# Performance work log

Hardware: AMD Instinct MI355X
Metric: run time of the kernel (lower is better)

Reference implementation:

```python
import jax, jax.numpy as jnp
import numpy as np

SPARSE_SHAPE = (41, 1600, 1408)  # (D, H, W), batch_size = 1
N_VOXELS = 200000
BN_EPS = 1e-3


def _kernel_offsets():
    # 27 offsets of a 3x3x3 kernel, padding=1 -> offsets in {-1,0,1}^3
    g = np.stack(np.meshgrid(*([np.arange(-1, 2)] * 3), indexing='ij'), axis=-1)
    return jnp.asarray(g.reshape(-1, 3), dtype=jnp.int32)  # (27, 3)


def _neighbor_map(coords):
    """Submanifold rulebook: for each active voxel and each of 27 offsets,
    index of the active neighbor voxel, or N (sentinel) if inactive/out-of-bounds."""
    D, H, W = SPARSE_SHAPE
    N = coords.shape[0]
    b, z, y, x = coords[:, 0], coords[:, 1], coords[:, 2], coords[:, 3]
    flat = ((b * D + z) * H + y) * W + x  # batch_size=1
    grid = jnp.full((D * H * W,), N, dtype=jnp.int32).at[flat].set(
        jnp.arange(N, dtype=jnp.int32))
    offs = _kernel_offsets()                      # (27, 3)
    nc = coords[:, None, 1:4] + offs[None]        # (N, 27, 3)
    lim = jnp.asarray([D, H, W], dtype=jnp.int32)
    valid = jnp.all((nc >= 0) & (nc < lim), axis=-1)  # (N, 27)
    nflat = ((b[:, None] * D + nc[..., 0]) * H + nc[..., 1]) * W + nc[..., 2]
    nbr = jnp.where(valid, grid[jnp.where(valid, nflat, 0)], N)
    return nbr  # (N, 27) int32, sentinel = N


def _subm_conv(features, nbr, w):
    # gather -> batched small GEMM -> (implicit) scatter back to same voxels
    pad = jnp.concatenate(
        [features, jnp.zeros((1, features.shape[1]), features.dtype)], axis=0)
    gathered = pad[nbr]                           # (N, 27, Cin)
    return jnp.einsum('nkc,kcd->nd', gathered, w)  # (N, Cout)


def _bn_relu(x, gamma, beta):
    # BatchNorm1d in train mode over the voxel (batch) dim, eps=1e-3
    mean = x.mean(axis=0)
    var = x.var(axis=0)
    return jax.nn.relu((x - mean) * jax.lax.rsqrt(var + BN_EPS) * gamma + beta)


def setup_inputs() -> dict:
    D, H, W = SPARSE_SHAPE
    total = D * H * W
    rng = np.random.default_rng(0)
    # unique active voxel locations
    flat = np.unique(rng.integers(0, total, size=N_VOXELS + 20000))
    rng.shuffle(flat)
    flat = flat[:N_VOXELS]
    assert flat.shape[0] == N_VOXELS
    z = flat // (H * W)
    y = (flat // W) % H
    x = flat % W
    b = np.zeros_like(z)
    coords = jnp.asarray(np.stack([b, z, y, x], axis=1), dtype=jnp.int32)

    key = jax.random.key(0)
    k0, k1, k2 = jax.random.split(key, 3)
    features = jax.random.uniform(k0, (N_VOXELS, 3), dtype=jnp.float32)
    w1 = jax.random.normal(k1, (27, 3, 16), dtype=jnp.float32) * 0.1
    w2 = jax.random.normal(k2, (27, 16, 16), dtype=jnp.float32) * 0.05
    return {
        'features': features, 'coords': coords,
        'w1': w1, 'gamma1': jnp.ones(16, jnp.float32), 'beta1': jnp.zeros(16, jnp.float32),
        'w2': w2, 'gamma2': jnp.ones(16, jnp.float32), 'beta2': jnp.zeros(16, jnp.float32),
    }


def reference(features, coords, w1, gamma1, beta1, w2, gamma2, beta2):
    nbr = _neighbor_map(coords)   # shared indice_key='subm1' -> reused by both convs
    h = _bn_relu(_subm_conv(features, nbr, w1), gamma1, beta1)
    h = _bn_relu(_subm_conv(h, nbr, w2), gamma2, beta2)
    return h
```

## Files before the change

kernel.cpp:

```cpp
#include <hip/hip_runtime.h>
#include <stdint.h>

#define SPARSE_D 41
#define SPARSE_H 1600
#define SPARSE_W 1408
#define BN_EPS 0.001f

static constexpr int NYB = SPARSE_H / 2;
static constexpr int NBUCKET = SPARSE_D * NYB;
static constexpr int NBS = (NBUCKET + 255) / 256;
static constexpr int PCAP = 12;


__global__ void k_insert(const int* __restrict__ coords, uint32_t* __restrict__ cnts,
                         uint32_t* __restrict__ slotarr, int N) {
    int n = blockIdx.x * blockDim.x + threadIdx.x;
    if (n >= N) return;
    int4 c4 = ((const int4*)coords)[n];
    int z = c4.y, y = c4.z;
    int b = z * NYB + (y >> 1);
    int slot = (int)atomicAdd(&cnts[b], 1u) + 1;
    slotarr[n] = ((uint32_t)b << 6) | (uint32_t)min(slot, 32);
}

__global__ void k_scanA(const uint32_t* __restrict__ cnts, uint32_t* __restrict__ bent2,
                        int* __restrict__ bsum, int NB) {
    __shared__ int ws[4];
    int b = blockIdx.x * 256 + threadIdx.x;
    int c = 0;
    if (b < NB) {
        uint32_t cv = cnts[b];
        bent2[(size_t)b * 32] = cv;
        c = min((int)cv, 31);
    }
    int s = c;
    #pragma unroll
    for (int off = 32; off; off >>= 1) s += __shfl_xor(s, off);
    int lane = threadIdx.x & 63, wid = threadIdx.x >> 6;
    if (lane == 0) ws[wid] = s;
    __syncthreads();
    if (threadIdx.x == 0) bsum[blockIdx.x] = ws[0] + ws[1] + ws[2] + ws[3];
}

__global__ void k_scanC(const uint32_t* __restrict__ cnts, const int* __restrict__ bsum,
                        int* __restrict__ base, int NB, int nbs) {
    __shared__ int ws[4];
    __shared__ int wsum[4];
    __shared__ int s_pref;
    int tid = threadIdx.x, lane = tid & 63, wid = tid >> 6;

    int pv = (tid < (int)blockIdx.x) ? bsum[tid] : 0;
    int ps = pv;
    #pragma unroll
    for (int off = 32; off; off >>= 1) ps += __shfl_xor(ps, off);
    if (lane == 0) ws[wid] = ps;
    __syncthreads();
    if (tid == 0) s_pref = ws[0] + ws[1] + ws[2] + ws[3];

    int b = blockIdx.x * 256 + tid;
    int c = (b < NB) ? min((int)cnts[b], 31) : 0;
    int inc = c;
    #pragma unroll
    for (int off = 1; off < 64; off <<= 1) {
        int t = __shfl_up(inc, off);
        if (lane >= off) inc += t;
    }
    if (lane == 63) wsum[wid] = inc;
    __syncthreads();
    if (tid == 0) {
        int r = 0;
        #pragma unroll
        for (int w = 0; w < 4; ++w) { int t = wsum[w]; wsum[w] = r; r += t; }
    }
    __syncthreads();
    int excl = s_pref + wsum[wid] + inc - c;
    if (b < NB) base[b] = excl;
    if ((int)blockIdx.x == nbs - 1 && tid == 255) {
        base[NB] = excl;
        base[NB + 1] = 0;
    }
}

__global__ void k_permute(const int* __restrict__ coords, const float* __restrict__ feat,
                          const uint32_t* __restrict__ slotarr, int* __restrict__ base,
                          uint32_t* __restrict__ bent2, uint32_t* __restrict__ czarr,
                          int* __restrict__ orig, float* __restrict__ featp, int NB, int N) {
    int n = blockIdx.x * blockDim.x + threadIdx.x;
    if (n >= N) return;
    uint32_t sv = slotarr[n];
    int b = (int)(sv >> 6), s = (int)(sv & 63u);
    int4 c4 = ((const int4*)coords)[n];
    int z = c4.y, y = c4.z, x = c4.w;
    int v;
    if (s <= 31) {
        v = base[b] + s - 1;
        bent2[(size_t)b * 32 + s] = ((uint32_t)(y & 1) << 29) | ((uint32_t)x << 18) | (uint32_t)v;
    } else {
        v = base[NB] + atomicAdd((uint32_t*)&base[NB + 1], 1u);
    }
    czarr[v] = ((uint32_t)z << 22) | ((uint32_t)y << 11) | (uint32_t)x;
    orig[v] = n;
    float f0 = feat[n * 3 + 0], f1 = feat[n * 3 + 1], f2 = feat[n * 3 + 2];
    ((float4*)featp)[v] = make_float4(f0, f1, f2, 0.f);
}

__device__ __forceinline__ int xcd_swz(int o, int nwg) {
    int q = nwg >> 3, r = nwg & 7;
    int x = o & 7, i = o >> 3;
    return (x < r ? x * (q + 1) : r * (q + 1) + (x - r) * q) + i;
}

__device__ __forceinline__ void stats_epilogue(const float acc[16],
                                               float* __restrict__ partials, int blk,
                                               float (*sred)[32]) {
    int lid = threadIdx.x & 63;
    int wid = threadIdx.x >> 6;
    #pragma unroll
    for (int d = 0; d < 16; ++d) {
        float v = acc[d];
        float v2 = v * v;
        #pragma unroll
        for (int off = 32; off; off >>= 1) {
            v += __shfl_xor(v, off);
            v2 += __shfl_xor(v2, off);
        }
        if (lid == 0) { sred[wid][d] = v; sred[wid][16 + d] = v2; }
    }
    __syncthreads();
    if (threadIdx.x < 32)
        partials[(size_t)blk * 32 + threadIdx.x] =
            sred[0][threadIdx.x] + sred[1][threadIdx.x] +
            sred[2][threadIdx.x] + sred[3][threadIdx.x];
}

__global__ void k_build_conv1(const uint32_t* __restrict__ czarr, const uint32_t* __restrict__ bent2,
                              const float* __restrict__ featp, const float* __restrict__ w1,
                              int* __restrict__ pcnt, uint32_t* __restrict__ pairs,
                              float* __restrict__ h1, float* __restrict__ partials, int N) {
    __shared__ float sred[4][32];
    __shared__ float sw1[27 * 52];
    for (int i = threadIdx.x; i < 27 * 48; i += 256)
        sw1[(i / 48) * 52 + (i % 48)] = w1[i];
    __syncthreads();

    int blk = xcd_swz(blockIdx.x, (int)gridDim.x);
    int v = blk * (int)blockDim.x + (int)threadIdx.x;
    float acc[16];
    #pragma unroll
    for (int d = 0; d < 16; ++d) acc[d] = 0.f;
    if (v < N) {
        uint32_t cz = czarr[v];
        int z = (int)(cz >> 22), y = (int)((cz >> 11) & 0x7FFu), x = (int)(cz & 0x7FFu);

        float4 f = ((const float4*)featp)[v];
        const float* wd = w1 + 13 * 48;
        #pragma unroll
        for (int d = 0; d < 16; ++d)
            acc[d] = fmaf(f.x, wd[d], fmaf(f.y, wd[16 + d], f.z * wd[32 + d]));

        int yb0 = (y - 1) >> 1;
        uint4 q0[6];
        int bix[6], mm[6];
        #pragma unroll
        for (int p = 0; p < 6; ++p) {
            int zz = z + p / 2 - 1;
            int yb = yb0 + (p & 1);
            bool ok = ((unsigned)zz < SPARSE_D) & ((unsigned)yb < NYB);
            int b = ok ? (zz * NYB + yb) : 0;
            bix[p] = b;
            q0[p] = *(const uint4*)&bent2[(size_t)b * 32];
            mm[p] = ok ? 1 : 0;
        }

        uint32_t lpairs[PCAP];
        int cnt = 0;
        #pragma unroll
        for (int p = 0; p < 6; ++p) {
            int m = mm[p] ? min((int)q0[p].x, 31) : 0;
            int yb = yb0 + (p & 1);
            int dzk = (p / 2) * 9;
            auto scan_entry = [&](uint32_t e, int slot) {
                if (slot > m) return;
                int ey = (yb << 1) + (int)(e >> 29);
                int ex = (int)((e >> 18) & 0x7FFu);
                int dy = ey - y, dx = ex - x;
                if ((unsigned)(dy + 1) > 2u || (unsigned)(dx + 1) > 2u) return;
                uint32_t idx = e & 0x3FFFFu;
                if (idx == (uint32_t)v) return;
                int k = dzk + (dy + 1) * 3 + (dx + 1);
                if (cnt < PCAP) lpairs[cnt] = ((uint32_t)k << 18) | idx;
                ++cnt;
            };
            scan_entry(q0[p].y, 1);
            scan_entry(q0[p].z, 2);
            scan_entry(q0[p].w, 3);
            for (int w = 4; w <= m; w += 4) {
                uint4 q = *(const uint4*)&bent2[(size_t)bix[p] * 32 + w];
                scan_entry(q.x, w);
                scan_entry(q.y, w + 1);
                scan_entry(q.z, w + 2);
                scan_entry(q.w, w + 3);
            }
        }
        cnt = min(cnt, PCAP);
        pcnt[v] = cnt;
        for (int c = 0; c < cnt; ++c) {
            uint32_t pr = lpairs[c];
            pairs[(size_t)c * N + v] = pr;
            int k = (int)(pr >> 18), idx = (int)(pr & 0x3FFFFu);
            float4 g = ((const float4*)featp)[idx];
            const float* wk = &sw1[k * 52];
            #pragma unroll
            for (int d = 0; d < 16; ++d)
                acc[d] = fmaf(g.x, wk[d], fmaf(g.y, wk[16 + d], fmaf(g.z, wk[32 + d], acc[d])));
        }
        float4* o = (float4*)&h1[(size_t)v * 16];
        o[0] = make_float4(acc[0], acc[1], acc[2], acc[3]);
        o[1] = make_float4(acc[4], acc[5], acc[6], acc[7]);
        o[2] = make_float4(acc[8], acc[9], acc[10], acc[11]);
        o[3] = make_float4(acc[12], acc[13], acc[14], acc[15]);
    }
    stats_epilogue(acc, partials, blk, sred);
}

__global__ void k_conv2(const float* __restrict__ h1, const int* __restrict__ pcnt,
                        const uint32_t* __restrict__ pairs, const float* __restrict__ w2,
                        const float* __restrict__ scsh1, const int* __restrict__ orig,
                        float* __restrict__ out, float* __restrict__ partials, int N) {
    __shared__ float sred[4][32];
    __shared__ float sc[16], sh[16];
    __shared__ float sw2[27 * 260];
    if (threadIdx.x < 16) { sc[threadIdx.x] = scsh1[threadIdx.x]; sh[threadIdx.x] = scsh1[16 + threadIdx.x]; }
    for (int i = threadIdx.x; i < 27 * 256; i += 256)
        sw2[(i >> 8) * 260 + (i & 255)] = w2[i];
    __syncthreads();

    int blk = xcd_swz(blockIdx.x, (int)gridDim.x);
    int v = blk * (int)blockDim.x + (int)threadIdx.x;
    float acc[16];
    #pragma unroll
    for (int d = 0; d < 16; ++d) acc[d] = 0.f;
    if (v < N) {
        float g[16];
        #pragma unroll
        for (int c = 0; c < 16; c += 4) {
            float4 t = *(const float4*)&h1[(size_t)v * 16 + c];
            g[c]     = fmaxf(fmaf(t.x, sc[c],     sh[c]),     0.f);
            g[c + 1] = fmaxf(fmaf(t.y, sc[c + 1], sh[c + 1]), 0.f);
            g[c + 2] = fmaxf(fmaf(t.z, sc[c + 2], sh[c + 2]), 0.f);
            g[c + 3] = fmaxf(fmaf(t.w, sc[c + 3], sh[c + 3]), 0.f);
        }
        {
            const float* w = w2 + 13 * 256;
            #pragma unroll
            for (int c = 0; c < 16; ++c)
                #pragma unroll
                for (int d = 0; d < 16; ++d)
                    acc[d] = fmaf(g[c], w[c * 16 + d], acc[d]);
        }
        int m = min(pcnt[v], PCAP);
        for (int cc = 0; cc < m; ++cc) {
            uint32_t pr = pairs[(size_t)cc * N + v];
            int k = (int)(pr >> 18), idx = (int)(pr & 0x3FFFFu);
            #pragma unroll
            for (int c = 0; c < 16; c += 4) {
                float4 t = *(const float4*)&h1[(size_t)idx * 16 + c];
                g[c]     = fmaxf(fmaf(t.x, sc[c],     sh[c]),     0.f);
                g[c + 1] = fmaxf(fmaf(t.y, sc[c + 1], sh[c + 1]), 0.f);
                g[c + 2] = fmaxf(fmaf(t.z, sc[c + 2], sh[c + 2]), 0.f);
                g[c + 3] = fmaxf(fmaf(t.w, sc[c + 3], sh[c + 3]), 0.f);
            }
            const float* wk = &sw2[k * 260];
            #pragma unroll
            for (int c = 0; c < 16; ++c)
                #pragma unroll
                for (int d = 0; d < 16; ++d)
                    acc[d] = fmaf(g[c], wk[c * 16 + d], acc[d]);
        }
        float4* o = (float4*)&out[(size_t)orig[v] * 16];
        o[0] = make_float4(acc[0], acc[1], acc[2], acc[3]);
        o[1] = make_float4(acc[4], acc[5], acc[6], acc[7]);
        o[2] = make_float4(acc[8], acc[9], acc[10], acc[11]);
        o[3] = make_float4(acc[12], acc[13], acc[14], acc[15]);
    }
    stats_epilogue(acc, partials, blk, sred);
}

__global__ void k_finalize(const float* __restrict__ partials, int nb,
                           const float* __restrict__ gamma, const float* __restrict__ beta,
                           float* __restrict__ scsh, float invN) {
    __shared__ float red[32][33];
    int ch = threadIdx.x & 31;
    int rg = threadIdx.x >> 5;
    float s0 = 0.f, s1 = 0.f, s2 = 0.f, s3 = 0.f;
    int j = rg;
    for (; j + 96 < nb; j += 128) {
        s0 += partials[(size_t)(j      ) * 32 + ch];
        s1 += partials[(size_t)(j + 32 ) * 32 + ch];
        s2 += partials[(size_t)(j + 64 ) * 32 + ch];
        s3 += partials[(size_t)(j + 96 ) * 32 + ch];
    }
    for (; j < nb; j += 32) s0 += partials[(size_t)j * 32 + ch];
    red[rg][ch] = (s0 + s1) + (s2 + s3);
    __syncthreads();
    if (threadIdx.x < 32) {
        float t = 0.f;
        #pragma unroll
        for (int r = 0; r < 32; ++r) t += red[r][threadIdx.x];
        red[0][threadIdx.x] = t;
    }
    __syncthreads();
    if (threadIdx.x < 16) {
        int d = threadIdx.x;
        float mean = red[0][d] * invN;
        float var = red[0][16 + d] * invN - mean * mean;
        float s2c = gamma[d] * rsqrtf(var + BN_EPS);
        scsh[d] = s2c;
        scsh[16 + d] = beta[d] - mean * s2c;
    }
}

__global__ void k_bnrelu4(float* __restrict__ x, const float* __restrict__ scsh, int nvec) {
    __shared__ float sc[16], sh[16];
    if (threadIdx.x < 16) { sc[threadIdx.x] = scsh[threadIdx.x]; sh[threadIdx.x] = scsh[16 + threadIdx.x]; }
    __syncthreads();
    int i = blockIdx.x * blockDim.x + threadIdx.x;
    if (i < nvec) {
        float4 v = ((float4*)x)[i];
        int c0 = (i & 3) * 4;
        v.x = fmaxf(fmaf(v.x, sc[c0 + 0], sh[c0 + 0]), 0.f);
        v.y = fmaxf(fmaf(v.y, sc[c0 + 1], sh[c0 + 1]), 0.f);
        v.z = fmaxf(fmaf(v.z, sc[c0 + 2], sh[c0 + 2]), 0.f);
        v.w = fmaxf(fmaf(v.w, sc[c0 + 3], sh[c0 + 3]), 0.f);
        ((float4*)x)[i] = v;
    }
}

extern "C" void kernel_launch(void* const* d_in, const int* in_sizes, int n_in,
                              void* d_out, int out_size, void* d_ws, size_t ws_size,
                              hipStream_t stream) {
    const float* feat   = (const float*)d_in[0];
    const int*   coords = (const int*)d_in[1];
    const float* w1     = (const float*)d_in[2];
    const float* gamma1 = (const float*)d_in[3];
    const float* beta1  = (const float*)d_in[4];
    const float* w2     = (const float*)d_in[5];
    const float* gamma2 = (const float*)d_in[6];
    const float* beta2  = (const float*)d_in[7];
    float* out = (float*)d_out;
    const int N = in_sizes[0] / 3;

    const int T = 256;
    const int nb = (N + T - 1) / T;
    const int nvec = N * 16 / 4;
    const int nbv = (nvec + T - 1) / T;
    const float invN = 1.f / (float)N;

    char* ws = (char*)d_ws;
    size_t off = 0;
    uint32_t* cnts  = (uint32_t*)(ws + off); off += ((size_t)NBUCKET * 4 + 63) & ~(size_t)63;
    int* base       = (int*)(ws + off);      off += ((size_t)(NBUCKET + 2) * 4 + 63) & ~(size_t)63;
    int* bsum       = (int*)(ws + off);      off += ((size_t)NBS * 4 + 63) & ~(size_t)63;
    uint32_t* bent2 = (uint32_t*)(ws + off); off += (size_t)NBUCKET * 32 * 4;
    uint32_t* slotarr = (uint32_t*)(ws + off); off += (size_t)N * 4;
    uint32_t* czarr = (uint32_t*)(ws + off); off += (size_t)N * 4;
    int* orig       = (int*)(ws + off);      off += (size_t)N * 4;
    int* pcnt       = (int*)(ws + off);      off += ((size_t)N * 4 + 63) & ~(size_t)63;
    uint32_t* pairs = (uint32_t*)(ws + off); off += (size_t)PCAP * N * 4;
    float* h1       = (float*)(ws + off);    off += (size_t)N * 16 * 4;
    float* featp    = (float*)(ws + off);    off += (size_t)N * 4 * 4;
    float* partials = (float*)(ws + off);    off += ((size_t)nb * 32 * 4 + 63) & ~(size_t)63;
    float* stats    = (float*)(ws + off);

    hipMemsetAsync(cnts, 0, (size_t)NBUCKET * 4, stream);
    k_insert<<<nb, T, 0, stream>>>(coords, cnts, slotarr, N);
    k_scanA<<<NBS, T, 0, stream>>>(cnts, bent2, bsum, NBUCKET);
    k_scanC<<<NBS, T, 0, stream>>>(cnts, bsum, base, NBUCKET, NBS);
    k_permute<<<nb, T, 0, stream>>>(coords, feat, slotarr, base, bent2, czarr, orig, featp,
                                    NBUCKET, N);
    k_build_conv1<<<nb, T, 0, stream>>>(czarr, bent2, featp, w1, pcnt, pairs, h1, partials, N);
    k_finalize<<<1, 1024, 0, stream>>>(partials, nb, gamma1, beta1, stats, invN);
    k_conv2<<<nb, T, 0, stream>>>(h1, pcnt, pairs, w2, stats, orig, out, partials, N);
    k_finalize<<<1, 1024, 0, stream>>>(partials, nb, gamma2, beta2, stats + 32, invN);
    k_bnrelu4<<<nbv, T, 0, stream>>>(out, stats + 32, nvec);
}
```

Measured before the change: 155.3 us.

## Fold BN finalize kernels into consumers via atomic 32-slot partial accumulation

Block statistics are now atomically accumulated into 32 striped slots, so the downstream kernels (conv2 and the final BN-ReLU) can reduce them in their prologue. This removes both single-block finalize launches and their serial tail. The coordinate and original-index arrays are packed into one uint2 array, and the stats buffers are zeroed by the existing memset. Costs are redundant per-block reduction of 1024 floats, atomic contention, and a final BN kernel with fewer blocks looping over a grid-stride.

```diff
diff --git a/kernel.cpp b/kernel.cpp
--- a/kernel.cpp
+++ b/kernel.cpp
@@ -83,8 +83,8 @@
 
 __global__ void k_permute(const int* __restrict__ coords, const float* __restrict__ feat,
                           const uint32_t* __restrict__ slotarr, int* __restrict__ base,
-                          uint32_t* __restrict__ bent2, uint32_t* __restrict__ czarr,
-                          int* __restrict__ orig, float* __restrict__ featp, int NB, int N) {
+                          uint32_t* __restrict__ bent2, uint2* __restrict__ vo,
+                          float* __restrict__ featp, int NB, int N) {
     int n = blockIdx.x * blockDim.x + threadIdx.x;
     if (n >= N) return;
     uint32_t sv = slotarr[n];
@@ -98,8 +98,8 @@
     } else {
         v = base[NB] + atomicAdd((uint32_t*)&base[NB + 1], 1u);
     }
-    czarr[v] = ((uint32_t)z << 22) | ((uint32_t)y << 11) | (uint32_t)x;
-    orig[v] = n;
+    uint32_t cz = ((uint32_t)z << 22) | ((uint32_t)y << 11) | (uint32_t)x;
+    vo[v] = make_uint2(cz, (uint32_t)n);
     float f0 = feat[n * 3 + 0], f1 = feat[n * 3 + 1], f2 = feat[n * 3 + 2];
     ((float4*)featp)[v] = make_float4(f0, f1, f2, 0.f);
 }
@@ -111,7 +111,7 @@
 }
 
 __device__ __forceinline__ void stats_epilogue(const float acc[16],
-                                               float* __restrict__ partials, int blk,
+                                               float* __restrict__ p, int blk,
                                                float (*sred)[32]) {
     int lid = threadIdx.x & 63;
     int wid = threadIdx.x >> 6;
@@ -128,15 +128,44 @@
     }
     __syncthreads();
     if (threadIdx.x < 32)
-        partials[(size_t)blk * 32 + threadIdx.x] =
-            sred[0][threadIdx.x] + sred[1][threadIdx.x] +
-            sred[2][threadIdx.x] + sred[3][threadIdx.x];
-}
-
-__global__ void k_build_conv1(const uint32_t* __restrict__ czarr, const uint32_t* __restrict__ bent2,
+        atomicAdd(&p[((blk & 31) << 5) + threadIdx.x],
+                  sred[0][threadIdx.x] + sred[1][threadIdx.x] +
+                  sred[2][threadIdx.x] + sred[3][threadIdx.x]);
+}
+
+__device__ __forceinline__ void reduce32(const float* __restrict__ p,
+                                         const float* __restrict__ gamma,
+                                         const float* __restrict__ beta,
+                                         float invN, float* __restrict__ sc,
+                                         float* __restrict__ sh) {
+    __shared__ float red[8][33];
+    int ch = threadIdx.x & 31, rg = threadIdx.x >> 5;
+    float s = p[(rg * 4 + 0) * 32 + ch] + p[(rg * 4 + 1) * 32 + ch] +
+              p[(rg * 4 + 2) * 32 + ch] + p[(rg * 4 + 3) * 32 + ch];
+    red[rg][ch] = s;
+    __syncthreads();
+    if (threadIdx.x < 32) {
+        float t = 0.f;
+        #pragma unroll
+        for (int r = 0; r < 8; ++r) t += red[r][threadIdx.x];
+        red[0][threadIdx.x] = t;
+    }
+    __syncthreads();
+    if (threadIdx.x < 16) {
+        int d = threadIdx.x;
+        float mean = red[0][d] * invN;
+        float var  = red[0][16 + d] * invN - mean * mean;
+        float s2c  = gamma[d] * rsqrtf(var + BN_EPS);
+        sc[d] = s2c;
+        sh[d] = beta[d] - mean * s2c;
+    }
+    __syncthreads();
+}
+
+__global__ void k_build_conv1(const uint2* __restrict__ vo, const uint32_t* __restrict__ bent2,
                               const float* __restrict__ featp, const float* __restrict__ w1,
                               int* __restrict__ pcnt, uint32_t* __restrict__ pairs,
-                              float* __restrict__ h1, float* __restrict__ partials, int N) {
+                              float* __restrict__ h1, float* __restrict__ p1, int N) {
     __shared__ float sred[4][32];
     __shared__ float sw1[27 * 52];
     for (int i = threadIdx.x; i < 27 * 48; i += 256)
@@ -149,7 +178,7 @@
     #pragma unroll
     for (int d = 0; d < 16; ++d) acc[d] = 0.f;
     if (v < N) {
-        uint32_t cz = czarr[v];
+        uint32_t cz = vo[v].x;
         int z = (int)(cz >> 22), y = (int)((cz >> 11) & 0x7FFu), x = (int)(cz & 0x7FFu);
 
         float4 f = ((const float4*)featp)[v];
@@ -220,20 +249,21 @@
         o[2] = make_float4(acc[8], acc[9], acc[10], acc[11]);
         o[3] = make_float4(acc[12], acc[13], acc[14], acc[15]);
     }
-    stats_epilogue(acc, partials, blk, sred);
+    stats_epilogue(acc, p1, blk, sred);
 }
 
 __global__ void k_conv2(const float* __restrict__ h1, const int* __restrict__ pcnt,
                         const uint32_t* __restrict__ pairs, const float* __restrict__ w2,
-                        const float* __restrict__ scsh1, const int* __restrict__ orig,
-                        float* __restrict__ out, float* __restrict__ partials, int N) {
+                        const float* __restrict__ p1,
+                        const float* __restrict__ gamma1, const float* __restrict__ beta1,
+                        float invN, const uint2* __restrict__ vo,
+                        float* __restrict__ out, float* __restrict__ p2, int N) {
     __shared__ float sred[4][32];
     __shared__ float sc[16], sh[16];
     __shared__ float sw2[27 * 260];
-    if (threadIdx.x < 16) { sc[threadIdx.x] = scsh1[threadIdx.x]; sh[threadIdx.x] = scsh1[16 + threadIdx.x]; }
     for (int i = threadIdx.x; i < 27 * 256; i += 256)
         sw2[(i >> 8) * 260 + (i & 255)] = w2[i];
-    __syncthreads();
+    reduce32(p1, gamma1, beta1, invN, sc, sh);
 
     int blk = xcd_swz(blockIdx.x, (int)gridDim.x);
     int v = blk * (int)blockDim.x + (int)threadIdx.x;
@@ -277,55 +307,22 @@
                 for (int d = 0; d < 16; ++d)
                     acc[d] = fmaf(g[c], wk[c * 16 + d], acc[d]);
         }
-        float4* o = (float4*)&out[(size_t)orig[v] * 16];
+        float4* o = (float4*)&out[(size_t)vo[v].y * 16];
         o[0] = make_float4(acc[0], acc[1], acc[2], acc[3]);
         o[1] = make_float4(acc[4], acc[5], acc[6], acc[7]);
         o[2] = make_float4(acc[8], acc[9], acc[10], acc[11]);
         o[3] = make_float4(acc[12], acc[13], acc[14], acc[15]);
     }
-    stats_epilogue(acc, partials, blk, sred);
-}
-
-__global__ void k_finalize(const float* __restrict__ partials, int nb,
-                           const float* __restrict__ gamma, const float* __restrict__ beta,
-                           float* __restrict__ scsh, float invN) {
-    __shared__ float red[32][33];
-    int ch = threadIdx.x & 31;
-    int rg = threadIdx.x >> 5;
-    float s0 = 0.f, s1 = 0.f, s2 = 0.f, s3 = 0.f;
-    int j = rg;
-    for (; j + 96 < nb; j += 128) {
-        s0 += partials[(size_t)(j      ) * 32 + ch];
-        s1 += partials[(size_t)(j + 32 ) * 32 + ch];
-        s2 += partials[(size_t)(j + 64 ) * 32 + ch];
-        s3 += partials[(size_t)(j + 96 ) * 32 + ch];
-    }
-    for (; j < nb; j += 32) s0 += partials[(size_t)j * 32 + ch];
-    red[rg][ch] = (s0 + s1) + (s2 + s3);
-    __syncthreads();
-    if (threadIdx.x < 32) {
-        float t = 0.f;
-        #pragma unroll
-        for (int r = 0; r < 32; ++r) t += red[r][threadIdx.x];
-        red[0][threadIdx.x] = t;
-    }
-    __syncthreads();
-    if (threadIdx.x < 16) {
-        int d = threadIdx.x;
-        float mean = red[0][d] * invN;
-        float var = red[0][16 + d] * invN - mean * mean;
-        float s2c = gamma[d] * rsqrtf(var + BN_EPS);
-        scsh[d] = s2c;
-        scsh[16 + d] = beta[d] - mean * s2c;
-    }
-}
-
-__global__ void k_bnrelu4(float* __restrict__ x, const float* __restrict__ scsh, int nvec) {
+    stats_epilogue(acc, p2, blk, sred);
+}
+
+__global__ void k_bnrelu_fin(float* __restrict__ x, const float* __restrict__ p2,
+                             const float* __restrict__ gamma2, const float* __restrict__ beta2,
+                             float invN, int nvec) {
     __shared__ float sc[16], sh[16];
-    if (threadIdx.x < 16) { sc[threadIdx.x] = scsh[threadIdx.x]; sh[threadIdx.x] = scsh[16 + threadIdx.x]; }
-    __syncthreads();
-    int i = blockIdx.x * blockDim.x + threadIdx.x;
-    if (i < nvec) {
+    reduce32(p2, gamma2, beta2, invN, sc, sh);
+    int G = (int)gridDim.x * (int)blockDim.x;
+    for (int i = blockIdx.x * blockDim.x + threadIdx.x; i < nvec; i += G) {
         float4 v = ((float4*)x)[i];
         int c0 = (i & 3) * 4;
         v.x = fmaxf(fmaf(v.x, sc[c0 + 0], sh[c0 + 0]), 0.f);
@@ -353,34 +350,32 @@
     const int T = 256;
     const int nb = (N + T - 1) / T;
     const int nvec = N * 16 / 4;
-    const int nbv = (nvec + T - 1) / T;
     const float invN = 1.f / (float)N;
 
     char* ws = (char*)d_ws;
     size_t off = 0;
-    uint32_t* cnts  = (uint32_t*)(ws + off); off += ((size_t)NBUCKET * 4 + 63) & ~(size_t)63;
+    uint32_t* cnts  = (uint32_t*)(ws + off); off += (size_t)NBUCKET * 4;
+    float* p1       = (float*)(ws + off);    off += 32 * 32 * 4;
+    float* p2       = (float*)(ws + off);    off += 32 * 32 * 4;
+    const size_t zbytes = off;
     int* base       = (int*)(ws + off);      off += ((size_t)(NBUCKET + 2) * 4 + 63) & ~(size_t)63;
     int* bsum       = (int*)(ws + off);      off += ((size_t)NBS * 4 + 63) & ~(size_t)63;
     uint32_t* bent2 = (uint32_t*)(ws + off); off += (size_t)NBUCKET * 32 * 4;
     uint32_t* slotarr = (uint32_t*)(ws + off); off += (size_t)N * 4;
-    uint32_t* czarr = (uint32_t*)(ws + off); off += (size_t)N * 4;
-    int* orig       = (int*)(ws + off);      off += (size_t)N * 4;
+    uint2* vo       = (uint2*)(ws + off);    off += (size_t)N * 8;
     int* pcnt       = (int*)(ws + off);      off += ((size_t)N * 4 + 63) & ~(size_t)63;
     uint32_t* pairs = (uint32_t*)(ws + off); off += (size_t)PCAP * N * 4;
     float* h1       = (float*)(ws + off);    off += (size_t)N * 16 * 4;
     float* featp    = (float*)(ws + off);    off += (size_t)N * 4 * 4;
-    float* partials = (float*)(ws + off);    off += ((size_t)nb * 32 * 4 + 63) & ~(size_t)63;
-    float* stats    = (float*)(ws + off);
-
-    hipMemsetAsync(cnts, 0, (size_t)NBUCKET * 4, stream);
+
+    hipMemsetAsync(cnts, 0, zbytes, stream);
     k_insert<<<nb, T, 0, stream>>>(coords, cnts, slotarr, N);
     k_scanA<<<NBS, T, 0, stream>>>(cnts, bent2, bsum, NBUCKET);
     k_scanC<<<NBS, T, 0, stream>>>(cnts, bsum, base, NBUCKET, NBS);
-    k_permute<<<nb, T, 0, stream>>>(coords, feat, slotarr, base, bent2, czarr, orig, featp,
+    k_permute<<<nb, T, 0, stream>>>(coords, feat, slotarr, base, bent2, vo, featp,
                                     NBUCKET, N);
-    k_build_conv1<<<nb, T, 0, stream>>>(czarr, bent2, featp, w1, pcnt, pairs, h1, partials, N);
-    k_finalize<<<1, 1024, 0, stream>>>(partials, nb, gamma1, beta1, stats, invN);
-    k_conv2<<<nb, T, 0, stream>>>(h1, pcnt, pairs, w2, stats, orig, out, partials, N);
-    k_finalize<<<1, 1024, 0, stream>>>(partials, nb, gamma2, beta2, stats + 32, invN);
-    k_bnrelu4<<<nbv, T, 0, stream>>>(out, stats + 32, nvec);
-}
+    k_build_conv1<<<nb, T, 0, stream>>>(vo, bent2, featp, w1, pcnt, pairs, h1, p1, N);
+    k_conv2<<<nb, T, 0, stream>>>(h1, pcnt, pairs, w2, p1, gamma1, beta1, invN,
+                                  vo, out, p2, N);
+    k_bnrelu_fin<<<nb, T, 0, stream>>>(out, p2, gamma2, beta2, invN, nvec);
+}
```

Result: faster. 150.1 us (-3.4%).
